# Kernel tuning notes

Measured on AMD Instinct MI355X. Metric: run time of the kernel, lower is better.

Reference implementation:

```python
import jax, jax.numpy as jnp
import numpy as np

V, L, D, DEMO, HID, N = 20000, 128, 256, 70, 1024, 2048


def setup_inputs() -> dict:
    key = jax.random.key(0)
    ks = jax.random.split(key, 16)
    s = 1.0 / np.sqrt(D)
    inp = {
        # learned parameters
        "E": jax.random.normal(ks[0], (V, D), jnp.float32) * 0.02,
        "Wq": jax.random.normal(ks[1], (D, D), jnp.float32) * s,
        "Wk": jax.random.normal(ks[2], (D, D), jnp.float32) * s,
        "Wv": jax.random.normal(ks[3], (D, D), jnp.float32) * s,
        "c_attn": jnp.ones((1,), jnp.float32) * 0.1,   # time_weight_net coefficient (attention decay)
        "c_pool": jnp.ones((1,), jnp.float32) * 0.5,   # history_repr Q_base-style pooling decay
        "W1": jax.random.normal(ks[4], (D + DEMO, HID), jnp.float32) * (1.0 / np.sqrt(D + DEMO)),
        "b1": jnp.zeros((HID,), jnp.float32),
        "W2": jax.random.normal(ks[5], (HID, 1), jnp.float32) * (1.0 / np.sqrt(HID)),
        "b2": jnp.zeros((1,), jnp.float32),
        # batched ragged task instances
        "demo": jax.random.normal(ks[6], (N, DEMO), jnp.float32),
        "hist_times": jax.random.uniform(ks[7], (N, L), jnp.float32) * 10.0,
        "event_time": jax.random.uniform(ks[8], (N,), jnp.float32) * 10.0 + 10.0,
        "labels": jax.random.randint(ks[9], (N,), 0, 2).astype(jnp.float32),
        "codes": jax.random.randint(ks[10], (N, L), 0, V),
        "lengths": jax.random.randint(ks[11], (N,), 1, L + 1).astype(jnp.int32),
    }
    return inp


def reference(E, Wq, Wk, Wv, c_attn, c_pool, W1, b1, W2, b2,
              demo, hist_times, event_time, labels, codes, lengths):
    POS_WEIGHT = 2.0
    NEG = jnp.float32(-1e9)
    mask = jnp.arange(L)[None, :] < lengths[:, None]            # [N, L] valid history positions

    emb = E[codes]                                              # [N, L, D] gather
    q = jnp.einsum('nld,de->nle', emb, Wq)
    k = jnp.einsum('nld,de->nle', emb, Wk)
    v = jnp.einsum('nld,de->nle', emb, Wv)

    # time-aware self-attention over each ragged history (masked)
    scores = jnp.einsum('nid,njd->nij', q, k) / jnp.sqrt(jnp.float32(D))
    dt = jnp.abs(hist_times[:, :, None] - hist_times[:, None, :])  # [N, L, L]
    scores = scores - c_attn[0] * dt
    scores = jnp.where(mask[:, None, :], scores, NEG)
    attn = jax.nn.softmax(scores, axis=-1)
    events = jnp.einsum('nij,njd->nid', attn, v)                # [N, L, D]

    # history_repr: time-decayed pooling toward event_time
    w = -c_pool[0] * (event_time[:, None] - hist_times)         # [N, L]
    w = jnp.where(mask, w, NEG)
    w = jax.nn.softmax(w, axis=-1)
    repr_ = jnp.einsum('nl,nld->nd', w, events)                 # [N, D]

    # disease/death classifier: demographics + history repr -> logit
    x = jnp.concatenate([demo, repr_], axis=-1)                 # [N, DEMO+D]
    h = jax.nn.relu(x @ W1 + b1)
    logit = (h @ W2 + b2)[:, 0]                                 # [N]

    # BCEWithLogitsLoss with pos_weight, averaged over valid predictions
    loss = -(POS_WEIGHT * labels * jax.nn.log_sigmoid(logit)
             + (1.0 - labels) * jax.nn.log_sigmoid(-logit))
    avg_loss = jnp.mean(loss)

    reg_loss = jnp.sum(c_attn ** 2) + jnp.sum(c_pool ** 2)      # time_weight_net.get_reg_loss()
    return avg_loss + reg_loss
```

## Files before the change

### kernel.cpp

```cpp
#include <hip/hip_runtime.h>
#include <hip/hip_bf16.h>
#include <math.h>
#include <stdint.h>

#define VV 20000
#define LL 128
#define DD 256
#define DEMO_ 70
#define HID_ 1024
#define NN 2048

typedef __attribute__((ext_vector_type(8))) short short8;
typedef __attribute__((ext_vector_type(4))) float f32x4;

__device__ __forceinline__ float bf2f(uint32_t u) {
    union { uint32_t u; float f; } c; c.u = u << 16; return c.f;
}
__device__ __forceinline__ uint32_t f2bf(float f) {
    union { float f; uint32_t u; } c; c.f = f;
    return (c.u + 0x7fffu + ((c.u >> 16) & 1u)) >> 16;
}

__device__ __forceinline__ int sw_off(int row, int col) {
    return (row << 8) + ((((col >> 3) ^ (row & 7)) << 3) | (col & 7));
}

__global__ __launch_bounds__(256) void k_pre(
    const float* __restrict__ Wq, const float* __restrict__ Wk,
    const float* __restrict__ Wv, const float* __restrict__ W1,
    const float* __restrict__ ca, const float* __restrict__ cp,
    const int* __restrict__ lens,
    unsigned short* __restrict__ Mxf, unsigned short* __restrict__ W1f,
    int* __restrict__ order, float* __restrict__ out)
{
    __shared__ float sm[DD];
    __shared__ float wvs[8][DD];
    __shared__ int cnt[9], off[9], cur[9];
    const int b = blockIdx.x, t = threadIdx.x;

    if (b < 256) {
        int e = b;
        sm[t] = Wq[(size_t)e * DD + t];
        __syncthreads();
        const float4* wk4 = (const float4*)(Wk + (size_t)t * DD);
        const float4* wq4 = (const float4*)sm;
        float4 acc = make_float4(0.f, 0.f, 0.f, 0.f);
        #pragma unroll 8
        for (int c = 0; c < DD / 4; ++c) {
            float4 a = wq4[c]; float4 bb = wk4[c];
            acc.x += a.x * bb.x; acc.y += a.y * bb.y;
            acc.z += a.z * bb.z; acc.w += a.w * bb.w;
        }
        float val = acc.x + acc.y + acc.z + acc.w;
        int frag = (e >> 4) * 8 + (t >> 5);
        int pos  = (((t >> 3) & 3) * 16 + (e & 15)) * 8 + (t & 7);
        Mxf[(size_t)frag * 512 + pos] = (unsigned short)f2bf(val);
    } else if (b < 384) {
        int f = b - 256, kg = f >> 2, hh = f & 3;
        #pragma unroll
        for (int r = 0; r < 8; ++r)
            wvs[r][t] = Wv[(size_t)(kg * 8 + r) * DD + t];
        __syncthreads();
        int h = hh * 256 + t;
        float acc[8];
        #pragma unroll
        for (int r = 0; r < 8; ++r) acc[r] = 0.f;
        #pragma unroll 4
        for (int n = 0; n < DD; ++n) {
            float a = W1[(size_t)(DEMO_ + n) * HID_ + h];
            #pragma unroll
            for (int r = 0; r < 8; ++r) acc[r] += wvs[r][n] * a;
        }
        #pragma unroll
        for (int r = 0; r < 8; ++r) {
            int k = DEMO_ + kg * 8 + r;
            int frag = (h >> 4) * 11 + (k >> 5);
            int pos  = (((k >> 3) & 3) * 16 + (h & 15)) * 8 + (k & 7);
            W1f[(size_t)frag * 512 + pos] = (unsigned short)f2bf(acc[r]);
        }
    } else if (b < 416) {
        int g = b - 384;
        for (int idx = g * 256 + t; idx < 96 * 1024; idx += 32 * 256) {
            int kk = idx >> 10, h = idx & 1023;
            int k = kk < DEMO_ ? kk : kk + 256;
            float val = kk < DEMO_ ? W1[(size_t)kk * HID_ + h] : 0.f;
            int frag = (h >> 4) * 11 + (k >> 5);
            int pos  = (((k >> 3) & 3) * 16 + (h & 15)) * 8 + (k & 7);
            W1f[(size_t)frag * 512 + pos] = (unsigned short)f2bf(val);
        }
    } else {
        if (t < 9) cnt[t] = 0;
        __syncthreads();
        for (int i = t; i < NN; i += 256)
            atomicAdd(&cnt[(lens[i] + 15) >> 4], 1);
        __syncthreads();
        if (t == 0) {
            int acc = 0;
            for (int k = 8; k >= 1; --k) { off[k] = acc; acc += cnt[k]; cur[k] = off[k]; }
            out[0] = ca[0] * ca[0] + cp[0] * cp[0];
        }
        __syncthreads();
        for (int i = t; i < NN; i += 256) {
            int key = (lens[i] + 15) >> 4;
            int pos = atomicAdd(&cur[key], 1);
            order[pos] = i;
        }
    }
}

__global__ __launch_bounds__(512, 4) void k_main(
    const float* __restrict__ E,
    const float* __restrict__ ht,  const float* __restrict__ evt_t,
    const int* __restrict__ codes, const int* __restrict__ lens,
    const float* __restrict__ ca_p, const float* __restrict__ cp_p,
    const unsigned short* __restrict__ Mxf,
    const int* __restrict__ order,
    unsigned short* __restrict__ Rbf)
{
    __shared__ __align__(16) unsigned short emb_u[LL * DD];
    __shared__ float times_s[LL];
    __shared__ int   codes_s[LL];
    __shared__ float w_s[LL];
    __shared__ float apart[8][LL];
    __shared__ float rp_part[8][DD];
    __shared__ float asum[LL];

    const int n = order[blockIdx.x];
    const int tid = threadIdx.x, wv = tid >> 6, ln = tid & 63;
    const int q = ln >> 4, m = ln & 15;
    const int len = lens[n];
    const int it_n = (len + 15) >> 4;
    const float ca = ca_p[0], cp = cp_p[0];
    const float evt = evt_t[n];

    short8 bB[2][8];
    #pragma unroll
    for (int nt = 0; nt < 2; ++nt)
        #pragma unroll
        for (int kk = 0; kk < 8; ++kk)
            bB[nt][kk] = *(const short8*)(Mxf + (size_t)((wv * 2 + nt) * 8 + kk) * 512 + ln * 8);

    if (tid < LL) {
        bool v = tid < len;
        times_s[tid] = v ? ht[(size_t)n * LL + tid] : 0.f;
        codes_s[tid] = v ? codes[(size_t)n * LL + tid] : 0;
    }
    if (wv == 0) {
        float t0 = (ln      < len) ? ht[(size_t)n * LL + ln]      : 0.f;
        float t1 = (ln + 64 < len) ? ht[(size_t)n * LL + ln + 64] : 0.f;
        float e0 = (ln      < len) ? __expf(cp * (t0 - evt)) : 0.f;
        float e1 = (ln + 64 < len) ? __expf(cp * (t1 - evt)) : 0.f;
        float smm = e0 + e1;
        for (int o = 32; o; o >>= 1) smm += __shfl_xor(smm, o, 64);
        float inv = 1.f / smm;
        if (ln      < len) w_s[ln]      = e0 * inv;
        if (ln + 64 < len) w_s[ln + 64] = e1 * inv;
    }
    __syncthreads();

    for (int l0 = wv; l0 < len; l0 += 32) {
        float4 v[4];
        #pragma unroll
        for (int u = 0; u < 4; ++u) {
            int l = l0 + u * 8;
            if (l < len)
                v[u] = ((const float4*)(E + (size_t)codes_s[l] * DD))[ln];
        }
        #pragma unroll
        for (int u = 0; u < 4; ++u) {
            int l = l0 + u * 8;
            if (l < len)
                *(uint2*)&emb_u[sw_off(l, 4 * ln)] =
                    make_uint2(f2bf(v[u].x) | (f2bf(v[u].y) << 16),
                               f2bf(v[u].z) | (f2bf(v[u].w) << 16));
        }
    }
    __syncthreads();

    short8 aC[8];
    for (int it = 0; it < it_n; ++it) {
        f32x4 h0 = (f32x4)0.f, h1 = (f32x4)0.f;
        #pragma unroll
        for (int kk = 0; kk < 8; ++kk) {
            short8 af = *(const short8*)&emb_u[sw_off(it * 16 + m, kk * 32 + q * 8)];
            if (it == wv) aC[kk] = af;
            h0 = __builtin_amdgcn_mfma_f32_16x16x32_bf16(af, bB[0][kk], h0, 0, 0, 0);
            h1 = __builtin_amdgcn_mfma_f32_16x16x32_bf16(af, bB[1][kk], h1, 0, 0, 0);
        }
        __syncthreads();
        #pragma unroll
        for (int r = 0; r < 4; ++r) {
            int row = it * 16 + q * 4 + r;
            emb_u[sw_off(row, wv * 32 + m)]      = (unsigned short)f2bf(h0[r]);
            emb_u[sw_off(row, wv * 32 + 16 + m)] = (unsigned short)f2bf(h1[r]);
        }
    }
    __syncthreads();

    if (wv < it_n) {
        f32x4 sac[8];
        #pragma unroll
        for (int jt = 0; jt < 8; ++jt) sac[jt] = (f32x4)0.f;
        for (int jt = 0; jt < it_n; ++jt) {
            #pragma unroll
            for (int kk = 0; kk < 8; ++kk) {
                short8 bH = *(const short8*)&emb_u[sw_off(jt * 16 + m, kk * 32 + q * 8)];
                sac[jt] = __builtin_amdgcn_mfma_f32_16x16x32_bf16(aC[kk], bH, sac[jt], 0, 0, 0);
            }
        }
        int i_base = wv * 16 + q * 4;
        float ti[4]; bool vR[4]; float rowsum[4];
        #pragma unroll
        for (int r = 0; r < 4; ++r) {
            vR[r] = (i_base + r) < len;
            ti[r] = times_s[i_base + r];
            rowsum[r] = 0.f;
        }
        for (int jt = 0; jt < it_n; ++jt) {
            int jcol = jt * 16 + m;
            bool vC = jcol < len;
            float tj = times_s[jcol];
            #pragma unroll
            for (int r = 0; r < 4; ++r) {
                float arg = sac[jt][r] * 0.0625f - ca * fabsf(ti[r] - tj);
                float p = (vR[r] && vC) ? __expf(arg) : 0.f;
                sac[jt][r] = p;
                rowsum[r] += p;
            }
        }
        #pragma unroll
        for (int r = 0; r < 4; ++r) {
            float s = rowsum[r];
            s += __shfl_xor(s, 1, 64); s += __shfl_xor(s, 2, 64);
            s += __shfl_xor(s, 4, 64); s += __shfl_xor(s, 8, 64);
            rowsum[r] = s;
        }
        float sc[4];
        #pragma unroll
        for (int r = 0; r < 4; ++r)
            sc[r] = (vR[r] && rowsum[r] > 0.f) ? w_s[i_base + r] / rowsum[r] : 0.f;
        for (int jt = 0; jt < it_n; ++jt) {
            float v = sc[0] * sac[jt][0] + sc[1] * sac[jt][1]
                    + sc[2] * sac[jt][2] + sc[3] * sac[jt][3];
            v += __shfl_xor(v, 16, 64);
            v += __shfl_xor(v, 32, 64);
            if (q == 0) apart[wv][jt * 16 + m] = v;
        }
    }
    __syncthreads();

    if (tid < LL) {
        float s = 0.f;
        for (int r = 0; r < it_n; ++r) s += apart[r][tid];
        asum[tid] = s;
    }
    __syncthreads();

    if (wv < it_n) {
        float aw = asum[wv * 16 + m];
        #pragma unroll
        for (int kk = 0; kk < 8; ++kk) {
            float v[8];
            #pragma unroll
            for (int j = 0; j < 8; ++j)
                v[j] = aw * bf2f((uint32_t)(unsigned short)aC[kk][j]);
            #pragma unroll
            for (int o = 1; o <= 8; o <<= 1)
                #pragma unroll
                for (int j = 0; j < 8; ++j)
                    v[j] += __shfl_xor(v[j], o, 64);
            if (m < 8)
                rp_part[wv][kk * 32 + q * 8 + m] = v[m];
        }
    }
    __syncthreads();
    if (tid < DD) {
        float r = 0.f;
        for (int t2 = 0; t2 < it_n; ++t2) r += rp_part[t2][tid];
        Rbf[(size_t)n * DD + tid] = (unsigned short)f2bf(r);
    }
}

__global__ __launch_bounds__(256, 2) void k_mlp(
    const float* __restrict__ demo, const float* __restrict__ labels,
    const float* __restrict__ b1,   const float* __restrict__ W2,
    const float* __restrict__ b2,
    const unsigned short* __restrict__ Rbf,
    const unsigned short* __restrict__ W1f,
    float* __restrict__ out)
{
    __shared__ __align__(16) unsigned short xs[16][360];
    __shared__ float W2s[HID_];
    __shared__ float b1s[HID_];
    __shared__ float wred[4][16];
    __shared__ float lred[16];

    const int tid = threadIdx.x, wv = tid >> 6, ln = tid & 63;
    const int q = ln >> 4, m = ln & 15;
    const int s0 = blockIdx.x * 16;

    #pragma unroll
    for (int hh = 0; hh < 4; ++hh) {
        W2s[tid + 256 * hh] = W2[tid + 256 * hh];
        b1s[tid + 256 * hh] = b1[tid + 256 * hh];
    }
    for (int s = 0; s < 16; ++s) {
        if (tid < DEMO_) xs[s][tid] = (unsigned short)f2bf(demo[(size_t)(s0 + s) * DEMO_ + tid]);
        xs[s][DEMO_ + tid] = Rbf[(size_t)(s0 + s) * DD + tid];
        if (tid < 34) xs[s][326 + tid] = 0;
    }
    __syncthreads();

    f32x4 cacc[16];
    #pragma unroll
    for (int ntl = 0; ntl < 16; ++ntl) cacc[ntl] = (f32x4)0.f;

    for (int kk = 0; kk < 11; ++kk) {
        short8 af = *(const short8*)&xs[m][kk * 32 + q * 8];
        #pragma unroll
        for (int ntl = 0; ntl < 16; ++ntl) {
            int frag = (wv * 16 + ntl) * 11 + kk;
            short8 bfd = *(const short8*)(W1f + (size_t)frag * 512 + ln * 8);
            cacc[ntl] = __builtin_amdgcn_mfma_f32_16x16x32_bf16(af, bfd, cacc[ntl], 0, 0, 0);
        }
    }

    float ls0 = 0.f, ls1 = 0.f, ls2 = 0.f, ls3 = 0.f;
    #pragma unroll
    for (int ntl = 0; ntl < 16; ++ntl) {
        int hl = wv * 256 + ntl * 16 + m;
        float bb = b1s[hl], w2v = W2s[hl];
        ls0 += fmaxf(cacc[ntl][0] + bb, 0.f) * w2v;
        ls1 += fmaxf(cacc[ntl][1] + bb, 0.f) * w2v;
        ls2 += fmaxf(cacc[ntl][2] + bb, 0.f) * w2v;
        ls3 += fmaxf(cacc[ntl][3] + bb, 0.f) * w2v;
    }
    #pragma unroll
    for (int o = 1; o <= 8; o <<= 1) {
        ls0 += __shfl_xor(ls0, o, 64); ls1 += __shfl_xor(ls1, o, 64);
        ls2 += __shfl_xor(ls2, o, 64); ls3 += __shfl_xor(ls3, o, 64);
    }
    if (m == 0) {
        wred[wv][q * 4 + 0] = ls0; wred[wv][q * 4 + 1] = ls1;
        wred[wv][q * 4 + 2] = ls2; wred[wv][q * 4 + 3] = ls3;
    }
    __syncthreads();
    if (tid < 16) {
        float z = wred[0][tid] + wred[1][tid] + wred[2][tid] + wred[3][tid] + b2[0];
        float y = labels[s0 + tid];
        float lg = log1pf(__expf(-fabsf(z)));
        float loss = 2.f * y * (fmaxf(-z, 0.f) + lg) + (1.f - y) * (fmaxf(z, 0.f) + lg);
        lred[tid] = loss;
    }
    __syncthreads();
    if (tid == 0) {
        float t = 0.f;
        #pragma unroll
        for (int i = 0; i < 16; ++i) t += lred[i];
        atomicAdd(out, t * (1.f / (float)NN));
    }
}

extern "C" void kernel_launch(void* const* d_in, const int* in_sizes, int n_in,
                              void* d_out, int out_size, void* d_ws, size_t ws_size,
                              hipStream_t stream) {
    const float* E      = (const float*)d_in[0];
    const float* Wq     = (const float*)d_in[1];
    const float* Wk     = (const float*)d_in[2];
    const float* Wv     = (const float*)d_in[3];
    const float* ca     = (const float*)d_in[4];
    const float* cp     = (const float*)d_in[5];
    const float* W1     = (const float*)d_in[6];
    const float* b1     = (const float*)d_in[7];
    const float* W2     = (const float*)d_in[8];
    const float* b2     = (const float*)d_in[9];
    const float* demo   = (const float*)d_in[10];
    const float* ht     = (const float*)d_in[11];
    const float* evt    = (const float*)d_in[12];
    const float* labels = (const float*)d_in[13];
    const int*   codes  = (const int*)d_in[14];
    const int*   lens   = (const int*)d_in[15];
    float* out = (float*)d_out;

    unsigned short* Mxf = (unsigned short*)d_ws;
    unsigned short* W1f = (unsigned short*)((char*)d_ws + 131072);
    unsigned short* Rbf = (unsigned short*)((char*)d_ws + 851968);
    int*            ord = (int*)((char*)d_ws + 1900544);

    hipLaunchKernelGGL(k_pre,  dim3(417), dim3(256), 0, stream,
                       Wq, Wk, Wv, W1, ca, cp, lens, Mxf, W1f, ord, out);
    hipLaunchKernelGGL(k_main, dim3(NN), dim3(512), 0, stream,
                       E, ht, evt, codes, lens, ca, cp, Mxf, ord, Rbf);
    hipLaunchKernelGGL(k_mlp,  dim3(NN / 16), dim3(256), 0, stream,
                       demo, labels, b1, W2, b2, Rbf, W1f, out);
}
```

Baseline: 251.5 us.

## Fuse MLP/loss into main kernel with persistent blocks handling four samples

The attention kernel now launches 512 blocks, and each block processes four samples taken at strided positions in the length-sorted order. That spreads long and short histories evenly across blocks. The separate MLP kernel is removed: each block runs the classifier and loss for its own four samples at the end, reusing shared memory. This saves one launch and a kernel boundary. In exchange, every block streams all of W1 to fill a 16-row MFMA tile with only 4 real rows, which multiplies weight traffic and wastes MFMA work. Padding rows of the embedding tile are now zero-filled so stale data from the previous sample does not leak in.

```diff
diff --git a/kernel.cpp b/kernel.cpp
--- a/kernel.cpp
+++ b/kernel.cpp
@@ -113,9 +113,14 @@
     const float* __restrict__ ht,  const float* __restrict__ evt_t,
     const int* __restrict__ codes, const int* __restrict__ lens,
     const float* __restrict__ ca_p, const float* __restrict__ cp_p,
+    const float* __restrict__ demo, const float* __restrict__ labels,
+    const float* __restrict__ b1,  const float* __restrict__ W2,
+    const float* __restrict__ b2,
     const unsigned short* __restrict__ Mxf,
+    const unsigned short* __restrict__ W1f,
     const int* __restrict__ order,
-    unsigned short* __restrict__ Rbf)
+    unsigned short* __restrict__ Rbf,
+    float* __restrict__ out)
 {
     __shared__ __align__(16) unsigned short emb_u[LL * DD];
     __shared__ float times_s[LL];
@@ -125,239 +130,234 @@
     __shared__ float rp_part[8][DD];
     __shared__ float asum[LL];
 
-    const int n = order[blockIdx.x];
+    const int b = blockIdx.x;
     const int tid = threadIdx.x, wv = tid >> 6, ln = tid & 63;
     const int q = ln >> 4, m = ln & 15;
-    const int len = lens[n];
-    const int it_n = (len + 15) >> 4;
     const float ca = ca_p[0], cp = cp_p[0];
-    const float evt = evt_t[n];
-
-    short8 bB[2][8];
-    #pragma unroll
-    for (int nt = 0; nt < 2; ++nt)
-        #pragma unroll
-        for (int kk = 0; kk < 8; ++kk)
-            bB[nt][kk] = *(const short8*)(Mxf + (size_t)((wv * 2 + nt) * 8 + kk) * 512 + ln * 8);
-
-    if (tid < LL) {
-        bool v = tid < len;
-        times_s[tid] = v ? ht[(size_t)n * LL + tid] : 0.f;
-        codes_s[tid] = v ? codes[(size_t)n * LL + tid] : 0;
-    }
-    if (wv == 0) {
-        float t0 = (ln      < len) ? ht[(size_t)n * LL + ln]      : 0.f;
-        float t1 = (ln + 64 < len) ? ht[(size_t)n * LL + ln + 64] : 0.f;
-        float e0 = (ln      < len) ? __expf(cp * (t0 - evt)) : 0.f;
-        float e1 = (ln + 64 < len) ? __expf(cp * (t1 - evt)) : 0.f;
-        float smm = e0 + e1;
-        for (int o = 32; o; o >>= 1) smm += __shfl_xor(smm, o, 64);
-        float inv = 1.f / smm;
-        if (ln      < len) w_s[ln]      = e0 * inv;
-        if (ln + 64 < len) w_s[ln + 64] = e1 * inv;
-    }
-    __syncthreads();
-
-    for (int l0 = wv; l0 < len; l0 += 32) {
-        float4 v[4];
-        #pragma unroll
-        for (int u = 0; u < 4; ++u) {
-            int l = l0 + u * 8;
-            if (l < len)
-                v[u] = ((const float4*)(E + (size_t)codes_s[l] * DD))[ln];
-        }
-        #pragma unroll
-        for (int u = 0; u < 4; ++u) {
-            int l = l0 + u * 8;
-            if (l < len)
-                *(uint2*)&emb_u[sw_off(l, 4 * ln)] =
-                    make_uint2(f2bf(v[u].x) | (f2bf(v[u].y) << 16),
-                               f2bf(v[u].z) | (f2bf(v[u].w) << 16));
-        }
-    }
-    __syncthreads();
-
-    short8 aC[8];
-    for (int it = 0; it < it_n; ++it) {
-        f32x4 h0 = (f32x4)0.f, h1 = (f32x4)0.f;
-        #pragma unroll
-        for (int kk = 0; kk < 8; ++kk) {
-            short8 af = *(const short8*)&emb_u[sw_off(it * 16 + m, kk * 32 + q * 8)];
-            if (it == wv) aC[kk] = af;
-            h0 = __builtin_amdgcn_mfma_f32_16x16x32_bf16(af, bB[0][kk], h0, 0, 0, 0);
-            h1 = __builtin_amdgcn_mfma_f32_16x16x32_bf16(af, bB[1][kk], h1, 0, 0, 0);
-        }
-        __syncthreads();
-        #pragma unroll
-        for (int r = 0; r < 4; ++r) {
-            int row = it * 16 + q * 4 + r;
-            emb_u[sw_off(row, wv * 32 + m)]      = (unsigned short)f2bf(h0[r]);
-            emb_u[sw_off(row, wv * 32 + 16 + m)] = (unsigned short)f2bf(h1[r]);
-        }
-    }
-    __syncthreads();
-
-    if (wv < it_n) {
-        f32x4 sac[8];
-        #pragma unroll
-        for (int jt = 0; jt < 8; ++jt) sac[jt] = (f32x4)0.f;
-        for (int jt = 0; jt < it_n; ++jt) {
+
+    for (int rep = 0; rep < 4; ++rep) {
+        const int n = order[b + 512 * rep];
+        const int len = lens[n];
+        const int it_n = (len + 15) >> 4;
+        const float evt = evt_t[n];
+
+        short8 bB[2][8];
+        #pragma unroll
+        for (int nt = 0; nt < 2; ++nt)
+            #pragma unroll
+            for (int kk = 0; kk < 8; ++kk)
+                bB[nt][kk] = *(const short8*)(Mxf + (size_t)((wv * 2 + nt) * 8 + kk) * 512 + ln * 8);
+
+        if (tid < LL) {
+            bool v = tid < len;
+            times_s[tid] = v ? ht[(size_t)n * LL + tid] : 0.f;
+            codes_s[tid] = v ? codes[(size_t)n * LL + tid] : 0;
+        }
+        if (wv == 0) {
+            float t0 = (ln      < len) ? ht[(size_t)n * LL + ln]      : 0.f;
+            float t1 = (ln + 64 < len) ? ht[(size_t)n * LL + ln + 64] : 0.f;
+            float e0 = (ln      < len) ? __expf(cp * (t0 - evt)) : 0.f;
+            float e1 = (ln + 64 < len) ? __expf(cp * (t1 - evt)) : 0.f;
+            float smm = e0 + e1;
+            for (int o = 32; o; o >>= 1) smm += __shfl_xor(smm, o, 64);
+            float inv = 1.f / smm;
+            if (ln      < len) w_s[ln]      = e0 * inv;
+            if (ln + 64 < len) w_s[ln + 64] = e1 * inv;
+        }
+        __syncthreads();
+
+        const int lmax = it_n * 16;
+        for (int l0 = wv; l0 < lmax; l0 += 32) {
+            float4 v[4];
+            #pragma unroll
+            for (int u = 0; u < 4; ++u) {
+                int l = l0 + u * 8;
+                v[u] = make_float4(0.f, 0.f, 0.f, 0.f);
+                if (l < len)
+                    v[u] = ((const float4*)(E + (size_t)codes_s[l] * DD))[ln];
+            }
+            #pragma unroll
+            for (int u = 0; u < 4; ++u) {
+                int l = l0 + u * 8;
+                if (l < lmax)
+                    *(uint2*)&emb_u[sw_off(l, 4 * ln)] =
+                        make_uint2(f2bf(v[u].x) | (f2bf(v[u].y) << 16),
+                                   f2bf(v[u].z) | (f2bf(v[u].w) << 16));
+            }
+        }
+        __syncthreads();
+
+        short8 aC[8];
+        for (int it = 0; it < it_n; ++it) {
+            f32x4 h0 = (f32x4)0.f, h1 = (f32x4)0.f;
             #pragma unroll
             for (int kk = 0; kk < 8; ++kk) {
-                short8 bH = *(const short8*)&emb_u[sw_off(jt * 16 + m, kk * 32 + q * 8)];
-                sac[jt] = __builtin_amdgcn_mfma_f32_16x16x32_bf16(aC[kk], bH, sac[jt], 0, 0, 0);
-            }
-        }
-        int i_base = wv * 16 + q * 4;
-        float ti[4]; bool vR[4]; float rowsum[4];
-        #pragma unroll
-        for (int r = 0; r < 4; ++r) {
-            vR[r] = (i_base + r) < len;
-            ti[r] = times_s[i_base + r];
-            rowsum[r] = 0.f;
-        }
-        for (int jt = 0; jt < it_n; ++jt) {
-            int jcol = jt * 16 + m;
-            bool vC = jcol < len;
-            float tj = times_s[jcol];
+                short8 af = *(const short8*)&emb_u[sw_off(it * 16 + m, kk * 32 + q * 8)];
+                if (it == wv) aC[kk] = af;
+                h0 = __builtin_amdgcn_mfma_f32_16x16x32_bf16(af, bB[0][kk], h0, 0, 0, 0);
+                h1 = __builtin_amdgcn_mfma_f32_16x16x32_bf16(af, bB[1][kk], h1, 0, 0, 0);
+            }
+            __syncthreads();
             #pragma unroll
             for (int r = 0; r < 4; ++r) {
-                float arg = sac[jt][r] * 0.0625f - ca * fabsf(ti[r] - tj);
-                float p = (vR[r] && vC) ? __expf(arg) : 0.f;
-                sac[jt][r] = p;
-                rowsum[r] += p;
-            }
-        }
-        #pragma unroll
-        for (int r = 0; r < 4; ++r) {
-            float s = rowsum[r];
-            s += __shfl_xor(s, 1, 64); s += __shfl_xor(s, 2, 64);
-            s += __shfl_xor(s, 4, 64); s += __shfl_xor(s, 8, 64);
-            rowsum[r] = s;
-        }
-        float sc[4];
-        #pragma unroll
-        for (int r = 0; r < 4; ++r)
-            sc[r] = (vR[r] && rowsum[r] > 0.f) ? w_s[i_base + r] / rowsum[r] : 0.f;
-        for (int jt = 0; jt < it_n; ++jt) {
-            float v = sc[0] * sac[jt][0] + sc[1] * sac[jt][1]
-                    + sc[2] * sac[jt][2] + sc[3] * sac[jt][3];
-            v += __shfl_xor(v, 16, 64);
-            v += __shfl_xor(v, 32, 64);
-            if (q == 0) apart[wv][jt * 16 + m] = v;
-        }
-    }
-    __syncthreads();
-
-    if (tid < LL) {
-        float s = 0.f;
-        for (int r = 0; r < it_n; ++r) s += apart[r][tid];
-        asum[tid] = s;
-    }
-    __syncthreads();
-
-    if (wv < it_n) {
-        float aw = asum[wv * 16 + m];
-        #pragma unroll
-        for (int kk = 0; kk < 8; ++kk) {
-            float v[8];
-            #pragma unroll
-            for (int j = 0; j < 8; ++j)
-                v[j] = aw * bf2f((uint32_t)(unsigned short)aC[kk][j]);
-            #pragma unroll
-            for (int o = 1; o <= 8; o <<= 1)
+                int row = it * 16 + q * 4 + r;
+                emb_u[sw_off(row, wv * 32 + m)]      = (unsigned short)f2bf(h0[r]);
+                emb_u[sw_off(row, wv * 32 + 16 + m)] = (unsigned short)f2bf(h1[r]);
+            }
+        }
+        __syncthreads();
+
+        if (wv < it_n) {
+            f32x4 sac[8];
+            #pragma unroll
+            for (int jt = 0; jt < 8; ++jt) sac[jt] = (f32x4)0.f;
+            for (int jt = 0; jt < it_n; ++jt) {
+                #pragma unroll
+                for (int kk = 0; kk < 8; ++kk) {
+                    short8 bH = *(const short8*)&emb_u[sw_off(jt * 16 + m, kk * 32 + q * 8)];
+                    sac[jt] = __builtin_amdgcn_mfma_f32_16x16x32_bf16(aC[kk], bH, sac[jt], 0, 0, 0);
+                }
+            }
+            int i_base = wv * 16 + q * 4;
+            float ti[4]; bool vR[4]; float rowsum[4];
+            #pragma unroll
+            for (int r = 0; r < 4; ++r) {
+                vR[r] = (i_base + r) < len;
+                ti[r] = times_s[i_base + r];
+                rowsum[r] = 0.f;
+            }
+            for (int jt = 0; jt < it_n; ++jt) {
+                int jcol = jt * 16 + m;
+                bool vC = jcol < len;
+                float tj = times_s[jcol];
+                #pragma unroll
+                for (int r = 0; r < 4; ++r) {
+                    float arg = sac[jt][r] * 0.0625f - ca * fabsf(ti[r] - tj);
+                    float p = (vR[r] && vC) ? __expf(arg) : 0.f;
+                    sac[jt][r] = p;
+                    rowsum[r] += p;
+                }
+            }
+            #pragma unroll
+            for (int r = 0; r < 4; ++r) {
+                float s = rowsum[r];
+                s += __shfl_xor(s, 1, 64); s += __shfl_xor(s, 2, 64);
+                s += __shfl_xor(s, 4, 64); s += __shfl_xor(s, 8, 64);
+                rowsum[r] = s;
+            }
+            float sc[4];
+            #pragma unroll
+            for (int r = 0; r < 4; ++r)
+                sc[r] = (vR[r] && rowsum[r] > 0.f) ? w_s[i_base + r] / rowsum[r] : 0.f;
+            for (int jt = 0; jt < it_n; ++jt) {
+                float v = sc[0] * sac[jt][0] + sc[1] * sac[jt][1]
+                        + sc[2] * sac[jt][2] + sc[3] * sac[jt][3];
+                v += __shfl_xor(v, 16, 64);
+                v += __shfl_xor(v, 32, 64);
+                if (q == 0) apart[wv][jt * 16 + m] = v;
+            }
+        }
+        __syncthreads();
+
+        if (tid < LL) {
+            float s = 0.f;
+            for (int r = 0; r < it_n; ++r) s += apart[r][tid];
+            asum[tid] = s;
+        }
+        __syncthreads();
+
+        if (wv < it_n) {
+            float aw = asum[wv * 16 + m];
+            #pragma unroll
+            for (int kk = 0; kk < 8; ++kk) {
+                float v[8];
                 #pragma unroll
                 for (int j = 0; j < 8; ++j)
-                    v[j] += __shfl_xor(v[j], o, 64);
-            if (m < 8)
-                rp_part[wv][kk * 32 + q * 8 + m] = v[m];
-        }
+                    v[j] = aw * bf2f((uint32_t)(unsigned short)aC[kk][j]);
+                #pragma unroll
+                for (int o = 1; o <= 8; o <<= 1)
+                    #pragma unroll
+                    for (int j = 0; j < 8; ++j)
+                        v[j] += __shfl_xor(v[j], o, 64);
+                if (m < 8)
+                    rp_part[wv][kk * 32 + q * 8 + m] = v[m];
+            }
+        }
+        __syncthreads();
+        if (tid < DD) {
+            float r = 0.f;
+            for (int t2 = 0; t2 < it_n; ++t2) r += rp_part[t2][tid];
+            Rbf[(size_t)n * DD + tid] = (unsigned short)f2bf(r);
+        }
+        __syncthreads();
     }
-    __syncthreads();
-    if (tid < DD) {
-        float r = 0.f;
-        for (int t2 = 0; t2 < it_n; ++t2) r += rp_part[t2][tid];
-        Rbf[(size_t)n * DD + tid] = (unsigned short)f2bf(r);
-    }
-}
-
-__global__ __launch_bounds__(256, 2) void k_mlp(
-    const float* __restrict__ demo, const float* __restrict__ labels,
-    const float* __restrict__ b1,   const float* __restrict__ W2,
-    const float* __restrict__ b2,
-    const unsigned short* __restrict__ Rbf,
-    const unsigned short* __restrict__ W1f,
-    float* __restrict__ out)
-{
-    __shared__ __align__(16) unsigned short xs[16][360];
-    __shared__ float W2s[HID_];
-    __shared__ float b1s[HID_];
-    __shared__ float wred[4][16];
-    __shared__ float lred[16];
-
-    const int tid = threadIdx.x, wv = tid >> 6, ln = tid & 63;
-    const int q = ln >> 4, m = ln & 15;
-    const int s0 = blockIdx.x * 16;
-
-    #pragma unroll
-    for (int hh = 0; hh < 4; ++hh) {
-        W2s[tid + 256 * hh] = W2[tid + 256 * hh];
-        b1s[tid + 256 * hh] = b1[tid + 256 * hh];
-    }
-    for (int s = 0; s < 16; ++s) {
-        if (tid < DEMO_) xs[s][tid] = (unsigned short)f2bf(demo[(size_t)(s0 + s) * DEMO_ + tid]);
-        xs[s][DEMO_ + tid] = Rbf[(size_t)(s0 + s) * DD + tid];
-        if (tid < 34) xs[s][326 + tid] = 0;
-    }
-    __syncthreads();
-
-    f32x4 cacc[16];
-    #pragma unroll
-    for (int ntl = 0; ntl < 16; ++ntl) cacc[ntl] = (f32x4)0.f;
-
-    for (int kk = 0; kk < 11; ++kk) {
-        short8 af = *(const short8*)&xs[m][kk * 32 + q * 8];
-        #pragma unroll
-        for (int ntl = 0; ntl < 16; ++ntl) {
-            int frag = (wv * 16 + ntl) * 11 + kk;
-            short8 bfd = *(const short8*)(W1f + (size_t)frag * 512 + ln * 8);
-            cacc[ntl] = __builtin_amdgcn_mfma_f32_16x16x32_bf16(af, bfd, cacc[ntl], 0, 0, 0);
-        }
-    }
-
-    float ls0 = 0.f, ls1 = 0.f, ls2 = 0.f, ls3 = 0.f;
-    #pragma unroll
-    for (int ntl = 0; ntl < 16; ++ntl) {
-        int hl = wv * 256 + ntl * 16 + m;
-        float bb = b1s[hl], w2v = W2s[hl];
-        ls0 += fmaxf(cacc[ntl][0] + bb, 0.f) * w2v;
-        ls1 += fmaxf(cacc[ntl][1] + bb, 0.f) * w2v;
-        ls2 += fmaxf(cacc[ntl][2] + bb, 0.f) * w2v;
-        ls3 += fmaxf(cacc[ntl][3] + bb, 0.f) * w2v;
-    }
-    #pragma unroll
-    for (int o = 1; o <= 8; o <<= 1) {
-        ls0 += __shfl_xor(ls0, o, 64); ls1 += __shfl_xor(ls1, o, 64);
-        ls2 += __shfl_xor(ls2, o, 64); ls3 += __shfl_xor(ls3, o, 64);
-    }
-    if (m == 0) {
-        wred[wv][q * 4 + 0] = ls0; wred[wv][q * 4 + 1] = ls1;
-        wred[wv][q * 4 + 2] = ls2; wred[wv][q * 4 + 3] = ls3;
-    }
-    __syncthreads();
-    if (tid < 16) {
-        float z = wred[0][tid] + wred[1][tid] + wred[2][tid] + wred[3][tid] + b2[0];
-        float y = labels[s0 + tid];
-        float lg = log1pf(__expf(-fabsf(z)));
-        float loss = 2.f * y * (fmaxf(-z, 0.f) + lg) + (1.f - y) * (fmaxf(z, 0.f) + lg);
-        lred[tid] = loss;
-    }
-    __syncthreads();
-    if (tid == 0) {
-        float t = 0.f;
-        #pragma unroll
-        for (int i = 0; i < 16; ++i) t += lred[i];
-        atomicAdd(out, t * (1.f / (float)NN));
+
+    {
+        unsigned short (*xs)[360] = (unsigned short(*)[360])emb_u;
+        float* wred = (float*)apart;
+        float* lred = asum;
+
+        {
+            int t2 = tid & 255, sh = tid >> 8;
+            for (int s = sh; s < 16; s += 2) {
+                unsigned short dv = 0, rv = 0;
+                if (s < 4) {
+                    int n_s = order[b + 512 * s];
+                    rv = Rbf[(size_t)n_s * DD + t2];
+                    if (t2 < DEMO_) dv = (unsigned short)f2bf(demo[(size_t)n_s * DEMO_ + t2]);
+                }
+                xs[s][DEMO_ + t2] = rv;
+                if (t2 < DEMO_) xs[s][t2] = dv;
+                if (t2 < 34) xs[s][326 + t2] = 0;
+            }
+        }
+        __syncthreads();
+
+        f32x4 cacc[8];
+        #pragma unroll
+        for (int ntl = 0; ntl < 8; ++ntl) cacc[ntl] = (f32x4)0.f;
+        for (int kk = 0; kk < 11; ++kk) {
+            short8 af = *(const short8*)&xs[m][kk * 32 + q * 8];
+            #pragma unroll
+            for (int ntl = 0; ntl < 8; ++ntl) {
+                int frag = (wv * 8 + ntl) * 11 + kk;
+                short8 bfd = *(const short8*)(W1f + (size_t)frag * 512 + ln * 8);
+                cacc[ntl] = __builtin_amdgcn_mfma_f32_16x16x32_bf16(af, bfd, cacc[ntl], 0, 0, 0);
+            }
+        }
+        float ls0 = 0.f, ls1 = 0.f, ls2 = 0.f, ls3 = 0.f;
+        #pragma unroll
+        for (int ntl = 0; ntl < 8; ++ntl) {
+            int h = (wv * 8 + ntl) * 16 + m;
+            float bb = b1[h], w2v = W2[h];
+            ls0 += fmaxf(cacc[ntl][0] + bb, 0.f) * w2v;
+            ls1 += fmaxf(cacc[ntl][1] + bb, 0.f) * w2v;
+            ls2 += fmaxf(cacc[ntl][2] + bb, 0.f) * w2v;
+            ls3 += fmaxf(cacc[ntl][3] + bb, 0.f) * w2v;
+        }
+        #pragma unroll
+        for (int o = 1; o <= 8; o <<= 1) {
+            ls0 += __shfl_xor(ls0, o, 64); ls1 += __shfl_xor(ls1, o, 64);
+            ls2 += __shfl_xor(ls2, o, 64); ls3 += __shfl_xor(ls3, o, 64);
+        }
+        if (ln == 0) {
+            wred[wv * 4 + 0] = ls0; wred[wv * 4 + 1] = ls1;
+            wred[wv * 4 + 2] = ls2; wred[wv * 4 + 3] = ls3;
+        }
+        __syncthreads();
+        if (tid < 4) {
+            float zz = b2[0];
+            #pragma unroll
+            for (int w = 0; w < 8; ++w) zz += wred[w * 4 + tid];
+            int n_s = order[b + 512 * tid];
+            float y = labels[n_s];
+            float lg = log1pf(__expf(-fabsf(zz)));
+            lred[tid] = 2.f * y * (fmaxf(-zz, 0.f) + lg)
+                      + (1.f - y) * (fmaxf(zz, 0.f) + lg);
+        }
+        __syncthreads();
+        if (tid == 0)
+            atomicAdd(out, (lred[0] + lred[1] + lred[2] + lred[3]) * (1.f / (float)NN));
     }
 }
 
@@ -389,8 +389,7 @@
 
     hipLaunchKernelGGL(k_pre,  dim3(417), dim3(256), 0, stream,
                        Wq, Wk, Wv, W1, ca, cp, lens, Mxf, W1f, ord, out);
-    hipLaunchKernelGGL(k_main, dim3(NN), dim3(512), 0, stream,
-                       E, ht, evt, codes, lens, ca, cp, Mxf, ord, Rbf);
-    hipLaunchKernelGGL(k_mlp,  dim3(NN / 16), dim3(256), 0, stream,
-                       demo, labels, b1, W2, b2, Rbf, W1f, out);
-}
+    hipLaunchKernelGGL(k_main, dim3(512), dim3(512), 0, stream,
+                       E, ht, evt, codes, lens, ca, cp, demo, labels,
+                       b1, W2, b2, Mxf, W1f, ord, Rbf, out);
+}
```

Measured after the change: 310.9 us. 23.6% more time.

## Split MLP hidden dimension across 4 blocks with atomic logit reduction

Applied to the files above, without the earlier changes.

The MLP kernel now launches a 2D grid: each block computes a 256-wide slice of the 1024 hidden units for 16 samples, atomically adds its partial logits to a global z buffer, and the last block per sample group (ticket counter) computes the BCE loss. This raises block count from 128 to 512 to better fill the GPU's CUs and cuts per-thread accumulator registers. Input staging is also vectorized. It adds global atomics, a threadfence/ticket protocol, and redundant loading of the x tile in each of the 4 blocks.

```diff
diff --git a/kernel.cpp b/kernel.cpp
--- a/kernel.cpp
+++ b/kernel.cpp
@@ -31,7 +31,8 @@
     const float* __restrict__ ca, const float* __restrict__ cp,
     const int* __restrict__ lens,
     unsigned short* __restrict__ Mxf, unsigned short* __restrict__ W1f,
-    int* __restrict__ order, float* __restrict__ out)
+    int* __restrict__ order, float* __restrict__ z,
+    int* __restrict__ tickets, float* __restrict__ out)
 {
     __shared__ float sm[DD];
     __shared__ float wvs[8][DD];
@@ -89,6 +90,8 @@
             W1f[(size_t)frag * 512 + pos] = (unsigned short)f2bf(val);
         }
     } else {
+        for (int i = t; i < NN; i += 256) z[i] = 0.f;
+        if (t < 128) tickets[t] = 0;
         if (t < 9) cnt[t] = 0;
         __syncthreads();
         for (int i = t; i < NN; i += 256)
@@ -281,45 +284,56 @@
     }
 }
 
-__global__ __launch_bounds__(256, 2) void k_mlp(
+__global__ __launch_bounds__(256) void k_mlp(
     const float* __restrict__ demo, const float* __restrict__ labels,
     const float* __restrict__ b1,   const float* __restrict__ W2,
     const float* __restrict__ b2,
     const unsigned short* __restrict__ Rbf,
     const unsigned short* __restrict__ W1f,
+    float* __restrict__ z, int* __restrict__ tickets,
     float* __restrict__ out)
 {
     __shared__ __align__(16) unsigned short xs[16][360];
-    __shared__ float W2s[HID_];
-    __shared__ float b1s[HID_];
+    __shared__ float W2s[256];
+    __shared__ float b1s[256];
     __shared__ float wred[4][16];
-    __shared__ float lred[16];
+    __shared__ int   lastflag;
 
     const int tid = threadIdx.x, wv = tid >> 6, ln = tid & 63;
     const int q = ln >> 4, m = ln & 15;
-    const int s0 = blockIdx.x * 16;
-
+    const int sg = blockIdx.x;
+    const int s0 = sg * 16;
+    const int by = blockIdx.y;
+    const int hbase = by * 256;
+
+    W2s[tid] = W2[hbase + tid];
+    b1s[tid] = b1[hbase + tid];
+    {
+        int sh = tid >> 6, lane = tid & 63;
+        for (int s = sh; s < 16; s += 4) {
+            int n_s = s0 + s;
+            const uint32_t* rsrc = (const uint32_t*)(Rbf + (size_t)n_s * DD);
+            ((uint32_t*)&xs[s][DEMO_])[lane]      = rsrc[lane];
+            ((uint32_t*)&xs[s][DEMO_])[lane + 64] = rsrc[lane + 64];
+            if (lane < 35) {
+                float2 d = ((const float2*)(demo + (size_t)n_s * DEMO_))[lane];
+                xs[s][2 * lane]     = (unsigned short)f2bf(d.x);
+                xs[s][2 * lane + 1] = (unsigned short)f2bf(d.y);
+            }
+            if (lane < 17) ((uint32_t*)&xs[s][326])[lane] = 0;
+        }
+    }
+    __syncthreads();
+
+    f32x4 cacc[4];
     #pragma unroll
-    for (int hh = 0; hh < 4; ++hh) {
-        W2s[tid + 256 * hh] = W2[tid + 256 * hh];
-        b1s[tid + 256 * hh] = b1[tid + 256 * hh];
-    }
-    for (int s = 0; s < 16; ++s) {
-        if (tid < DEMO_) xs[s][tid] = (unsigned short)f2bf(demo[(size_t)(s0 + s) * DEMO_ + tid]);
-        xs[s][DEMO_ + tid] = Rbf[(size_t)(s0 + s) * DD + tid];
-        if (tid < 34) xs[s][326 + tid] = 0;
-    }
-    __syncthreads();
-
-    f32x4 cacc[16];
-    #pragma unroll
-    for (int ntl = 0; ntl < 16; ++ntl) cacc[ntl] = (f32x4)0.f;
+    for (int ntl = 0; ntl < 4; ++ntl) cacc[ntl] = (f32x4)0.f;
 
     for (int kk = 0; kk < 11; ++kk) {
         short8 af = *(const short8*)&xs[m][kk * 32 + q * 8];
         #pragma unroll
-        for (int ntl = 0; ntl < 16; ++ntl) {
-            int frag = (wv * 16 + ntl) * 11 + kk;
+        for (int ntl = 0; ntl < 4; ++ntl) {
+            int frag = (by * 16 + wv * 4 + ntl) * 11 + kk;
             short8 bfd = *(const short8*)(W1f + (size_t)frag * 512 + ln * 8);
             cacc[ntl] = __builtin_amdgcn_mfma_f32_16x16x32_bf16(af, bfd, cacc[ntl], 0, 0, 0);
         }
@@ -327,8 +341,8 @@
 
     float ls0 = 0.f, ls1 = 0.f, ls2 = 0.f, ls3 = 0.f;
     #pragma unroll
-    for (int ntl = 0; ntl < 16; ++ntl) {
-        int hl = wv * 256 + ntl * 16 + m;
+    for (int ntl = 0; ntl < 4; ++ntl) {
+        int hl = wv * 64 + ntl * 16 + m;
         float bb = b1s[hl], w2v = W2s[hl];
         ls0 += fmaxf(cacc[ntl][0] + bb, 0.f) * w2v;
         ls1 += fmaxf(cacc[ntl][1] + bb, 0.f) * w2v;
@@ -345,19 +359,28 @@
         wred[wv][q * 4 + 2] = ls2; wred[wv][q * 4 + 3] = ls3;
     }
     __syncthreads();
-    if (tid < 16) {
-        float z = wred[0][tid] + wred[1][tid] + wred[2][tid] + wred[3][tid] + b2[0];
-        float y = labels[s0 + tid];
-        float lg = log1pf(__expf(-fabsf(z)));
-        float loss = 2.f * y * (fmaxf(-z, 0.f) + lg) + (1.f - y) * (fmaxf(z, 0.f) + lg);
-        lred[tid] = loss;
-    }
-    __syncthreads();
+    if (tid < 16)
+        atomicAdd(&z[s0 + tid], wred[0][tid] + wred[1][tid] + wred[2][tid] + wred[3][tid]);
+    __syncthreads();
+
     if (tid == 0) {
-        float t = 0.f;
-        #pragma unroll
-        for (int i = 0; i < 16; ++i) t += lred[i];
-        atomicAdd(out, t * (1.f / (float)NN));
+        __threadfence();
+        int ticket = atomicAdd(&tickets[sg], 1);
+        lastflag = (ticket == 3);
+    }
+    __syncthreads();
+    if (lastflag && wv == 0) {
+        float loss = 0.f;
+        if (ln < 16) {
+            float zz = atomicAdd(&z[s0 + ln], 0.f) + b2[0];
+            float y = labels[s0 + ln];
+            float lg = log1pf(__expf(-fabsf(zz)));
+            loss = 2.f * y * (fmaxf(-zz, 0.f) + lg)
+                 + (1.f - y) * (fmaxf(zz, 0.f) + lg);
+        }
+        #pragma unroll
+        for (int o = 1; o <= 8; o <<= 1) loss += __shfl_xor(loss, o, 64);
+        if (ln == 0) atomicAdd(out, loss * (1.f / (float)NN));
     }
 }
 
@@ -385,12 +408,14 @@
     unsigned short* Mxf = (unsigned short*)d_ws;
     unsigned short* W1f = (unsigned short*)((char*)d_ws + 131072);
     unsigned short* Rbf = (unsigned short*)((char*)d_ws + 851968);
-    int*            ord = (int*)((char*)d_ws + 1900544);
+    float*          zar = (float*)((char*)d_ws + 1900544);
+    int*            ord = (int*)((char*)d_ws + 1908736);
+    int*            tks = (int*)((char*)d_ws + 1916928);
 
     hipLaunchKernelGGL(k_pre,  dim3(417), dim3(256), 0, stream,
-                       Wq, Wk, Wv, W1, ca, cp, lens, Mxf, W1f, ord, out);
+                       Wq, Wk, Wv, W1, ca, cp, lens, Mxf, W1f, ord, zar, tks, out);
     hipLaunchKernelGGL(k_main, dim3(NN), dim3(512), 0, stream,
                        E, ht, evt, codes, lens, ca, cp, Mxf, ord, Rbf);
-    hipLaunchKernelGGL(k_mlp,  dim3(NN / 16), dim3(256), 0, stream,
-                       demo, labels, b1, W2, b2, Rbf, W1f, out);
-}
+    hipLaunchKernelGGL(k_mlp,  dim3(NN / 16, 4), dim3(256), 0, stream,
+                       demo, labels, b1, W2, b2, Rbf, W1f, zar, tks, out);
+}
```

Result: faster. 226.5 us (-10.0%).
